# Performance work log

Hardware: AMD Instinct MI355X
Metric: run time of the kernel (lower is better)

Reference implementation:

```python
import jax, jax.numpy as jnp
import numpy as np

DIM = 768
NUM_HEADS = 12
HEAD_DIM = DIM // NUM_HEADS
SCALE = HEAD_DIM ** -0.5
SPARSITY = 0.1


def setup_inputs() -> dict:
    key = jax.random.key(0)
    ks = jax.random.split(key, 6)
    B, N, C = 2, 4096, DIM
    s = 0.02
    return {
        "x": jax.random.normal(ks[0], (B, N, C), dtype=jnp.float32),
        "Wq": jax.random.normal(ks[1], (C, C), dtype=jnp.float32) * s,
        "Wk": jax.random.normal(ks[2], (C, C), dtype=jnp.float32) * s,
        "Wv": jax.random.normal(ks[3], (C, C), dtype=jnp.float32) * s,
        "Wp": jax.random.normal(ks[4], (C, C), dtype=jnp.float32) * s,
        "bp": jax.random.normal(ks[5], (C,), dtype=jnp.float32) * s,
    }


def reference(x, Wq, Wk, Wv, Wp, bp):
    B, N, C = x.shape
    H, D = NUM_HEADS, HEAD_DIM
    # nn.Linear: y = x @ W.T ; here W is stored as (out, in) equivalent -> use W.T
    q = (x @ Wq.T).reshape(B, N, H, D).transpose(0, 2, 1, 3)  # [B,H,N,D]
    k = (x @ Wk.T).reshape(B, N, H, D).transpose(0, 2, 1, 3)
    v = (x @ Wv.T).reshape(B, N, H, D).transpose(0, 2, 1, 3)
    attn = jnp.einsum("bhnd,bhmd->bhnm", q, k) * SCALE  # [B,H,N,N]
    attn = jax.nn.softmax(attn, axis=-1)
    num_keep = max(1, int(N * SPARSITY))
    topk_vals, topk_idx = jax.lax.top_k(attn, num_keep)  # [B,H,N,K]
    bi = jnp.arange(B)[:, None, None, None]
    hi = jnp.arange(H)[None, :, None, None]
    ni = jnp.arange(N)[None, None, :, None]
    sparse_attn = jnp.zeros_like(attn).at[bi, hi, ni, topk_idx].set(topk_vals)
    out = jnp.einsum("bhnm,bhmd->bhnd", sparse_attn, v)  # [B,H,N,D]
    out = out.transpose(0, 2, 1, 3).reshape(B, N, C)
    return out @ Wp.T + bp
```

## Files before the change

kernel.cpp:

```cpp
#include <hip/hip_runtime.h>


typedef unsigned short u16;
typedef unsigned int   u32;
typedef float    f32x4 __attribute__((ext_vector_type(4)));
typedef _Float16 f16x8 __attribute__((ext_vector_type(8)));
typedef u16      u16x8 __attribute__((ext_vector_type(8)));
typedef u16      u16x4 __attribute__((ext_vector_type(4)));
typedef u32      u32x4 __attribute__((ext_vector_type(4)));

#define NHEADS 12
#define SEQ    4096
#define DIMC   768
#define HDIM   64
#define KKEEP  409

__device__ __forceinline__ f32x4 mfma16(f16x8 a, f16x8 b, f32x4 c) {
  return __builtin_amdgcn_mfma_f32_16x16x32_f16(a, b, c, 0, 0, 0);
}
__device__ __forceinline__ u16 f2h_bits(float f) {
  return __builtin_bit_cast(u16, (_Float16)f);
}

__global__ __launch_bounds__(256) void cast_f32_to_f16(const float* __restrict__ in,
                                                       u16* __restrict__ out, int n4) {
  int i = blockIdx.x * 256 + threadIdx.x;
  if (i >= n4) return;
  float4 v = ((const float4*)in)[i];
  u16x4 o;
  o[0] = f2h_bits(v.x); o[1] = f2h_bits(v.y); o[2] = f2h_bits(v.z); o[3] = f2h_bits(v.w);
  ((u16x4*)out)[i] = o;
}

template<int MODE>
__global__ __launch_bounds__(256) void gemm_nt(const u16* __restrict__ A, const u16* __restrict__ B,
                                               float scale, const float* __restrict__ bias,
                                               void* __restrict__ dstv) {
  __shared__ __align__(16) u16 As[128 * 64];
  __shared__ __align__(16) u16 Bs[128 * 64];
  const int tid  = threadIdx.x;
  const int lane = tid & 63, wave = tid >> 6;
  const int l15 = lane & 15, l4 = lane >> 4;
  const int row0 = blockIdx.x * 128, col0 = blockIdx.y * 128;
  const int wr = (wave >> 1) * 64, wc = (wave & 1) * 64;
  f32x4 acc[4][4];
#pragma unroll
  for (int i = 0; i < 4; i++)
#pragma unroll
    for (int j = 0; j < 4; j++) acc[i][j] = f32x4{0.f, 0.f, 0.f, 0.f};

  for (int k0 = 0; k0 < DIMC; k0 += 64) {
#pragma unroll
    for (int i = 0; i < 4; i++) {
      int id = tid + i * 256;
      int r = id >> 3, c = id & 7;
      f16x8 va = *(const f16x8*)(A + (size_t)(row0 + r) * DIMC + k0 + c * 8);
      f16x8 vb = *(const f16x8*)(B + (size_t)(col0 + r) * DIMC + k0 + c * 8);
      *(f16x8*)(As + r * 64 + ((c ^ (r & 7)) << 3)) = va;
      *(f16x8*)(Bs + r * 64 + ((c ^ (r & 7)) << 3)) = vb;
    }
    __syncthreads();
#pragma unroll
    for (int ks = 0; ks < 2; ++ks) {
      f16x8 af[4], bfr[4];
#pragma unroll
      for (int i = 0; i < 4; i++) {
        int r = wr + i * 16 + l15;
        int c = ks * 4 + l4;
        af[i] = *(const f16x8*)(As + r * 64 + ((c ^ (r & 7)) << 3));
        int r2 = wc + i * 16 + l15;
        bfr[i] = *(const f16x8*)(Bs + r2 * 64 + ((c ^ (r2 & 7)) << 3));
      }
#pragma unroll
      for (int i = 0; i < 4; i++)
#pragma unroll
        for (int j = 0; j < 4; j++) acc[i][j] = mfma16(af[i], bfr[j], acc[i][j]);
    }
    __syncthreads();
  }

#pragma unroll
  for (int i = 0; i < 4; i++) {
#pragma unroll
    for (int j = 0; j < 4; j++) {
      int rowb = row0 + wr + i * 16 + (l4 << 2);
      int col  = col0 + wc + j * 16 + l15;
      if (MODE == 2) {
        float* dst = (float*)dstv;
        float bv = bias[col];
#pragma unroll
        for (int jj = 0; jj < 4; jj++)
          dst[(size_t)(rowb + jj) * DIMC + col] = acc[i][j][jj] + bv;
      } else if (MODE == 0) {
        u16* dst = (u16*)dstv;
        int hh = col >> 6, d = col & 63;
#pragma unroll
        for (int jj = 0; jj < 4; jj++) {
          int row = rowb + jj;
          int bb = row >> 12, n = row & 4095;
          dst[(((size_t)bb * NHEADS + hh) * SEQ + n) * HDIM + d] = f2h_bits(acc[i][j][jj] * scale);
        }
      } else {
        u16* dst = (u16*)dstv;
        int hh = col >> 6, d = col & 63;
        int bb = rowb >> 12, nb = rowb & 4095;
        u16x4 pack;
#pragma unroll
        for (int jj = 0; jj < 4; jj++) pack[jj] = f2h_bits(acc[i][j][jj] * scale);
        *(u16x4*)(dst + (((size_t)bb * NHEADS + hh) * HDIM + d) * SEQ + nb) = pack;
      }
    }
  }
}

__global__ __launch_bounds__(1024, 4) void attn_kernel(const u16* __restrict__ Q, const u16* __restrict__ Kb,
                                                       const u16* __restrict__ Vt, u16* __restrict__ Ob) {
  __shared__ __align__(16) u16 S[16 * 4096];
  __shared__ float zbuf[16][64];
  __shared__ float invZs[16];
  const int tid  = threadIdx.x;
  const int lane = tid & 63, wave = tid >> 6;
  const int l15 = lane & 15, l4 = lane >> 4;
  const int h = blockIdx.y, b = blockIdx.z;
  const int bh = b * NHEADS + h;
  const int q0 = blockIdx.x * 16;
  const u16* Qh = Q  + ((size_t)bh * SEQ + q0) * HDIM;
  const u16* Kh = Kb + (size_t)bh * SEQ * HDIM;
  const u16* Vh = Vt + (size_t)bh * HDIM * SEQ;

  f16x8 qa0 = *(const f16x8*)(Qh + l15 * HDIM + l4 * 8);
  f16x8 qa1 = *(const f16x8*)(Qh + l15 * HDIM + 32 + l4 * 8);

  const int m0base = wave * 256;
  float zp = 0.f;
  {
    const u16* kptr = Kh + (size_t)(m0base + l15) * HDIM + l4 * 8;
    f16x8 kb0 = *(const f16x8*)kptr;
    f16x8 kb1 = *(const f16x8*)(kptr + 32);
#pragma unroll 1
    for (int t = 0; t < 16; ++t) {
      f16x8 cur0 = kb0, cur1 = kb1;
      if (t < 15) {
        const u16* kpn = Kh + (size_t)(m0base + (t + 1) * 16 + l15) * HDIM + l4 * 8;
        kb0 = *(const f16x8*)kpn;
        kb1 = *(const f16x8*)(kpn + 32);
      }
      f32x4 acc = f32x4{0.f, 0.f, 0.f, 0.f};
      acc = mfma16(cur0, qa0, acc);
      acc = mfma16(cur1, qa1, acc);
      int m0 = m0base + t * 16;
      int g = (m0 >> 3) + (l4 >> 1);
      u16x4 pack;
#pragma unroll
      for (int j = 0; j < 4; j++) {
        float e = __expf(fminf(acc[j], 11.0f));
        zp += e;
        pack[j] = f2h_bits(e);
      }
      *(u16x4*)(S + (l15 << 12) + ((g ^ (l15 & 7)) << 3) + ((l4 & 1) << 2)) = pack;
    }
  }
  zbuf[l15][(wave << 2) + l4] = zp;
  __syncthreads();

  {
    const u32 rbase = (u32)wave << 12;
    const u32 rx = (u32)(wave & 7) << 3;
    const u32 H = 0x80008000u;
    u32 X[8][4];
#pragma unroll
    for (int cc = 0; cc < 8; ++cc) {
      u32 c = (u32)cc * 64 + lane;
      u32x4 v = *(const u32x4*)(S + rbase + ((c << 3) ^ rx));
#pragma unroll
      for (int p = 0; p < 4; p++) X[cc][p] = v[p] | H;
    }
    u32 lo = 0, hi = 0x7FFFu, c1 = 0;
    while (lo < hi) {
      u32 mid = (lo + hi) >> 1;
      u32 M1 = (mid + 1) * 0x10001u;
      u32 pc = 0;
#pragma unroll
      for (int cc = 0; cc < 8; ++cc)
#pragma unroll
        for (int p = 0; p < 4; p++) {
          u32 d = X[cc][p] - M1;
          pc += (d & H) >> 15;
        }
#pragma unroll
      for (int o = 32; o; o >>= 1) pc += __shfl_xor(pc, o);
      u32 cnt = (pc & 0xFFFFu) + (pc >> 16);
      if (cnt < KKEEP) { hi = mid; c1 = cnt; } else lo = mid + 1;
    }
    const u32 t = lo;
    float z = zbuf[wave][lane];
#pragma unroll
    for (int o = 32; o; o >>= 1) z += __shfl_xor(z, o);
    if (lane == 0) invZs[wave] = 1.f / z;
    const int r = KKEEP - (int)c1;

    const u32 M1t = (t + 1) * 0x10001u;
    const u32 M0t = t * 0x10001u;
    int run = 0;
#pragma unroll 1
    for (int cc = 0; cc < 8; ++cc) {
      u32 g1[4], eqm[4], eqany = 0;
#pragma unroll
      for (int p = 0; p < 4; p++) {
        u32 x = X[cc][p];
        g1[p] = (x - M1t) & H;
        u32 g0 = (x - M0t) & H;
        eqm[p] = g0 ^ g1[p];
        eqany |= eqm[p];
      }
      u32 c = (u32)cc * 64 + lane;
      u32* dst = (u32*)(S + rbase + ((c << 3) ^ rx));
      if (!__any(eqany != 0)) {
        u32x4 o;
#pragma unroll
        for (int p = 0; p < 4; p++) {
          u32 m = g1[p] | (g1[p] - (g1[p] >> 15));
          o[p] = X[cc][p] & m & 0x7FFF7FFFu;
        }
        *(u32x4*)dst = o;
      } else {
        u32 s = 0;
#pragma unroll
        for (int p = 0; p < 4; p++) s += eqm[p] >> 15;
        int ec = (int)((s & 0xFFFFu) + (s >> 16));
        int inc = ec;
#pragma unroll
        for (int o = 1; o < 64; o <<= 1) { int pfx = __shfl_up(inc, o); if (lane >= o) inc += pfx; }
        int rk = run + inc - ec;
        run += __shfl(inc, 63);
        u32x4 o;
#pragma unroll
        for (int p = 0; p < 4; p++) {
          u32 x = X[cc][p];
          u32 glo = (g1[p] >> 15) & 1u, ghi = g1[p] >> 31;
          u32 elo = (eqm[p] >> 15) & 1u, ehi = eqm[p] >> 31;
          u32 klo = glo | (elo & (rk < r ? 1u : 0u)); rk += (int)elo;
          u32 khi = ghi | (ehi & (rk < r ? 1u : 0u)); rk += (int)ehi;
          o[p] = x & ((klo ? 0xFFFFu : 0u) | (khi ? 0xFFFF0000u : 0u)) & 0x7FFF7FFFu;
        }
        *(u32x4*)dst = o;
      }
    }
  }
  __syncthreads();

  f32x4 oacc[4];
#pragma unroll
  for (int dt = 0; dt < 4; dt++) oacc[dt] = f32x4{0.f, 0.f, 0.f, 0.f};
#pragma unroll 1
  for (int ks = 0; ks < 8; ++ks) {
    int mb = wave * 256 + ks * 32;
    u32 c = (u32)(mb >> 3) + l4;
    f16x8 pa = *(const f16x8*)(S + (l15 << 12) + (((c ^ (l15 & 7))) << 3));
#pragma unroll
    for (int dt = 0; dt < 4; ++dt) {
      const u16* vp = Vh + (size_t)(dt * 16 + l15) * SEQ + mb + l4 * 8;
      f16x8 vb = *(const f16x8*)vp;
      oacc[dt] = mfma16(pa, vb, oacc[dt]);
    }
  }
  __syncthreads();
  float* Op = (float*)S;
#pragma unroll
  for (int dt = 0; dt < 4; dt++)
#pragma unroll
    for (int j = 0; j < 4; j++)
      Op[(wave * 16 + l4 * 4 + j) * 65 + dt * 16 + l15] = oacc[dt][j];
  __syncthreads();
  {
    int row = tid >> 6, d = tid & 63;
    float v = 0.f;
#pragma unroll
    for (int w = 0; w < 16; ++w) v += Op[(w * 16 + row) * 65 + d];
    v *= invZs[row];
    Ob[((size_t)b * SEQ + q0 + row) * DIMC + h * HDIM + d] = f2h_bits(v);
  }
}

extern "C" void kernel_launch(void* const* d_in, const int* in_sizes, int n_in,
                              void* d_out, int out_size, void* d_ws, size_t ws_size,
                              hipStream_t stream) {
  const float* x  = (const float*)d_in[0];
  const float* Wq = (const float*)d_in[1];
  const float* Wk = (const float*)d_in[2];
  const float* Wv = (const float*)d_in[3];
  const float* Wp = (const float*)d_in[4];
  const float* bp = (const float*)d_in[5];
  float* out = (float*)d_out;

  const size_t M = 2 * (size_t)SEQ;
  const size_t XB = M * DIMC * 2;
  const size_t WB = (size_t)DIMC * DIMC * 2;

  char* w = (char*)d_ws;
  u16* xb   = (u16*)w; w += XB;
  u16* Wqb  = (u16*)w; w += WB;
  u16* Wkb  = (u16*)w; w += WB;
  u16* Wvb  = (u16*)w; w += WB;
  u16* Wpb  = (u16*)w; w += WB;
  u16* Qb   = (u16*)w; w += XB;
  u16* Kbuf = (u16*)w; w += XB;
  u16* Vtb  = (u16*)w; w += XB;
  u16* Obuf = (u16*)w; w += XB;

  cast_f32_to_f16<<<6144, 256, 0, stream>>>(x,  xb,  (int)(M * DIMC / 4));
  cast_f32_to_f16<<<576,  256, 0, stream>>>(Wq, Wqb, (int)(WB / 8));
  cast_f32_to_f16<<<576,  256, 0, stream>>>(Wk, Wkb, (int)(WB / 8));
  cast_f32_to_f16<<<576,  256, 0, stream>>>(Wv, Wvb, (int)(WB / 8));
  cast_f32_to_f16<<<576,  256, 0, stream>>>(Wp, Wpb, (int)(WB / 8));

  dim3 gg(64, 6);
  gemm_nt<0><<<gg, 256, 0, stream>>>(xb, Wqb, 0.125f, nullptr, Qb);
  gemm_nt<0><<<gg, 256, 0, stream>>>(xb, Wkb, 1.0f,   nullptr, Kbuf);
  gemm_nt<1><<<gg, 256, 0, stream>>>(xb, Wvb, 1.0f,   nullptr, Vtb);

  attn_kernel<<<dim3(256, NHEADS, 2), 1024, 0, stream>>>(Qb, Kbuf, Vtb, Obuf);

  gemm_nt<2><<<gg, 256, 0, stream>>>(Obuf, Wpb, 1.0f, bp, out);
}
```

Measured before the change: 1.282 ms.

## Halve attention query rows per block and use DPP wave reductions

Each attention block now handles 8 query rows with 8 waves of 512 keys each, down from 16 rows with 16 waves. This halves the shared-memory score buffer, so more blocks fit per CU and scheduling granularity is finer. The cost is that half of each 16-row MFMA tile is wasted, and K and V are streamed twice as often per query. The shuffle-xor reductions in the top-k binary search and the softmax normaliser are replaced with DPP row and broadcast adds plus readlane, to cut reduction latency inside the search loop.

```diff
diff --git a/kernel.cpp b/kernel.cpp
--- a/kernel.cpp
+++ b/kernel.cpp
@@ -14,12 +14,30 @@
 #define DIMC   768
 #define HDIM   64
 #define KKEEP  409
+#define QROWS  8
 
 __device__ __forceinline__ f32x4 mfma16(f16x8 a, f16x8 b, f32x4 c) {
   return __builtin_amdgcn_mfma_f32_16x16x32_f16(a, b, c, 0, 0, 0);
 }
 __device__ __forceinline__ u16 f2h_bits(float f) {
   return __builtin_bit_cast(u16, (_Float16)f);
+}
+
+__device__ __forceinline__ u32 wred_add_u32(u32 x) {
+  x += (u32)__builtin_amdgcn_update_dpp(0, (int)x, 0x111, 0xF, 0xF, true);
+  x += (u32)__builtin_amdgcn_update_dpp(0, (int)x, 0x112, 0xF, 0xF, true);
+  x += (u32)__builtin_amdgcn_update_dpp(0, (int)x, 0x114, 0xF, 0xF, true);
+  x += (u32)__builtin_amdgcn_update_dpp(0, (int)x, 0x118, 0xF, 0xF, true);
+  x += (u32)__builtin_amdgcn_update_dpp(0, (int)x, 0x142, 0xF, 0xF, true);
+  x += (u32)__builtin_amdgcn_update_dpp(0, (int)x, 0x143, 0xF, 0xF, true);
+  return (u32)__builtin_amdgcn_readlane((int)x, 63);
+}
+__device__ __forceinline__ float wred_add_f32(float x) {
+#define _DPPF(ctrl) x += __builtin_bit_cast(float, __builtin_amdgcn_update_dpp( \
+      0, __builtin_bit_cast(int, x), ctrl, 0xF, 0xF, true));
+  _DPPF(0x111) _DPPF(0x112) _DPPF(0x114) _DPPF(0x118) _DPPF(0x142) _DPPF(0x143)
+#undef _DPPF
+  return __builtin_bit_cast(float, __builtin_amdgcn_readlane(__builtin_bit_cast(int, x), 63));
 }
 
 __global__ __launch_bounds__(256) void cast_f32_to_f16(const float* __restrict__ in,
@@ -113,34 +131,35 @@
   }
 }
 
-__global__ __launch_bounds__(1024, 4) void attn_kernel(const u16* __restrict__ Q, const u16* __restrict__ Kb,
-                                                       const u16* __restrict__ Vt, u16* __restrict__ Ob) {
-  __shared__ __align__(16) u16 S[16 * 4096];
-  __shared__ float zbuf[16][64];
-  __shared__ float invZs[16];
+__global__ __launch_bounds__(512, 4) void attn_kernel(const u16* __restrict__ Q, const u16* __restrict__ Kb,
+                                                      const u16* __restrict__ Vt, u16* __restrict__ Ob) {
+  __shared__ __align__(16) u16 S[QROWS * 4096];
+  __shared__ float zbuf[QROWS][32];
+  __shared__ float invZs[QROWS];
   const int tid  = threadIdx.x;
   const int lane = tid & 63, wave = tid >> 6;
   const int l15 = lane & 15, l4 = lane >> 4;
+  const int r7  = l15 & 7;
   const int h = blockIdx.y, b = blockIdx.z;
   const int bh = b * NHEADS + h;
-  const int q0 = blockIdx.x * 16;
+  const int q0 = blockIdx.x * QROWS;
   const u16* Qh = Q  + ((size_t)bh * SEQ + q0) * HDIM;
   const u16* Kh = Kb + (size_t)bh * SEQ * HDIM;
   const u16* Vh = Vt + (size_t)bh * HDIM * SEQ;
 
-  f16x8 qa0 = *(const f16x8*)(Qh + l15 * HDIM + l4 * 8);
-  f16x8 qa1 = *(const f16x8*)(Qh + l15 * HDIM + 32 + l4 * 8);
-
-  const int m0base = wave * 256;
+  f16x8 qa0 = *(const f16x8*)(Qh + r7 * HDIM + l4 * 8);
+  f16x8 qa1 = *(const f16x8*)(Qh + r7 * HDIM + 32 + l4 * 8);
+
+  const int m0base = wave * 512;
   float zp = 0.f;
   {
     const u16* kptr = Kh + (size_t)(m0base + l15) * HDIM + l4 * 8;
     f16x8 kb0 = *(const f16x8*)kptr;
     f16x8 kb1 = *(const f16x8*)(kptr + 32);
 #pragma unroll 1
-    for (int t = 0; t < 16; ++t) {
+    for (int t = 0; t < 32; ++t) {
       f16x8 cur0 = kb0, cur1 = kb1;
-      if (t < 15) {
+      if (t < 31) {
         const u16* kpn = Kh + (size_t)(m0base + (t + 1) * 16 + l15) * HDIM + l4 * 8;
         kb0 = *(const f16x8*)kpn;
         kb1 = *(const f16x8*)(kpn + 32);
@@ -157,10 +176,11 @@
         zp += e;
         pack[j] = f2h_bits(e);
       }
-      *(u16x4*)(S + (l15 << 12) + ((g ^ (l15 & 7)) << 3) + ((l4 & 1) << 2)) = pack;
-    }
-  }
-  zbuf[l15][(wave << 2) + l4] = zp;
+      if (l15 < 8)
+        *(u16x4*)(S + (l15 << 12) + ((g ^ r7) << 3) + ((l4 & 1) << 2)) = pack;
+    }
+  }
+  if (l15 < 8) zbuf[l15][(wave << 2) + l4] = zp;
   __syncthreads();
 
   {
@@ -187,15 +207,13 @@
           u32 d = X[cc][p] - M1;
           pc += (d & H) >> 15;
         }
-#pragma unroll
-      for (int o = 32; o; o >>= 1) pc += __shfl_xor(pc, o);
-      u32 cnt = (pc & 0xFFFFu) + (pc >> 16);
+      u32 s = wred_add_u32(pc);
+      u32 cnt = (s & 0xFFFFu) + (s >> 16);
       if (cnt < KKEEP) { hi = mid; c1 = cnt; } else lo = mid + 1;
     }
     const u32 t = lo;
-    float z = zbuf[wave][lane];
-#pragma unroll
-    for (int o = 32; o; o >>= 1) z += __shfl_xor(z, o);
+    float z = (lane < 32) ? zbuf[wave][lane] : 0.f;
+    z = wred_add_f32(z);
     if (lane == 0) invZs[wave] = 1.f / z;
     const int r = KKEEP - (int)c1;
 
@@ -253,10 +271,10 @@
 #pragma unroll
   for (int dt = 0; dt < 4; dt++) oacc[dt] = f32x4{0.f, 0.f, 0.f, 0.f};
 #pragma unroll 1
-  for (int ks = 0; ks < 8; ++ks) {
-    int mb = wave * 256 + ks * 32;
+  for (int ks = 0; ks < 16; ++ks) {
+    int mb = wave * 512 + ks * 32;
     u32 c = (u32)(mb >> 3) + l4;
-    f16x8 pa = *(const f16x8*)(S + (l15 << 12) + (((c ^ (l15 & 7))) << 3));
+    f16x8 pa = *(const f16x8*)(S + (r7 << 12) + ((c ^ r7) << 3));
 #pragma unroll
     for (int dt = 0; dt < 4; ++dt) {
       const u16* vp = Vh + (size_t)(dt * 16 + l15) * SEQ + mb + l4 * 8;
@@ -266,17 +284,19 @@
   }
   __syncthreads();
   float* Op = (float*)S;
-#pragma unroll
-  for (int dt = 0; dt < 4; dt++)
-#pragma unroll
-    for (int j = 0; j < 4; j++)
-      Op[(wave * 16 + l4 * 4 + j) * 65 + dt * 16 + l15] = oacc[dt][j];
+  if (l4 < 2) {
+#pragma unroll
+    for (int dt = 0; dt < 4; dt++)
+#pragma unroll
+      for (int j = 0; j < 4; j++)
+        Op[(wave * 8 + l4 * 4 + j) * 65 + dt * 16 + l15] = oacc[dt][j];
+  }
   __syncthreads();
   {
     int row = tid >> 6, d = tid & 63;
     float v = 0.f;
 #pragma unroll
-    for (int w = 0; w < 16; ++w) v += Op[(w * 16 + row) * 65 + d];
+    for (int w = 0; w < 8; ++w) v += Op[(w * 8 + row) * 65 + d];
     v *= invZs[row];
     Ob[((size_t)b * SEQ + q0 + row) * DIMC + h * HDIM + d] = f2h_bits(v);
   }
@@ -319,7 +339,7 @@
   gemm_nt<0><<<gg, 256, 0, stream>>>(xb, Wkb, 1.0f,   nullptr, Kbuf);
   gemm_nt<1><<<gg, 256, 0, stream>>>(xb, Wvb, 1.0f,   nullptr, Vtb);
 
-  attn_kernel<<<dim3(256, NHEADS, 2), 1024, 0, stream>>>(Qb, Kbuf, Vtb, Obuf);
+  attn_kernel<<<dim3(SEQ / QROWS, NHEADS, 2), 512, 0, stream>>>(Qb, Kbuf, Vtb, Obuf);
 
   gemm_nt<2><<<gg, 256, 0, stream>>>(Obuf, Wpb, 1.0f, bp, out);
 }
```

Measured after the change: 1.584 ms. +23.6%, slower.
